# Performance work log

Measured on AMD Instinct MI355X. Metric: run time of the kernel, lower is better.

The kernel has to match this reference:

```python
import jax, jax.numpy as jnp
import numpy as np

N = 100000   # nodes
E = 400000   # merged window edges
L = 100000   # label edges to decode
DIN = 128
H = 128
NL = 2       # GCN layers
RATIO = 0.8
DOUT = 1


def setup_inputs() -> dict:
    key = jax.random.key(0)
    ks = jax.random.split(key, 24)
    def nrm(k, shape, fan):
        return (jax.random.normal(k, shape, jnp.float32) / np.sqrt(fan)).astype(jnp.float32)
    inp = {
        'x': jax.random.normal(ks[0], (N, DIN), jnp.float32),
        'edge_index': jax.random.randint(ks[1], (2, E), 0, N, jnp.int64) if jax.config.jax_enable_x64 else jax.random.randint(ks[1], (2, E), 0, N, jnp.int32),
        'edge_label_index': jax.random.randint(ks[2], (2, L), 0, N, jnp.int32),
        'edge_time': jax.random.uniform(ks[3], (E,), jnp.float32),
        'previous_state': jax.random.normal(ks[4], (N, H), jnp.float32),
        # mlp_transform: Linear(DIN,H)+ReLU
        'w_mlp': nrm(ks[5], (DIN, H), DIN), 'b_mlp': jnp.zeros((H,), jnp.float32),
        # TimeEncode: cos(Linear(1,H)(t))
        'w_time': nrm(ks[6], (H,), 1), 'b_time': jnp.zeros((H,), jnp.float32),
        # Sampling MLP: Linear(3H,H)+ReLU, Linear(H,1)
        'w_s1': nrm(ks[7], (3 * H, H), 3 * H), 'b_s1': jnp.zeros((H,), jnp.float32),
        'w_s2': nrm(ks[8], (H, 1), H), 'b_s2': jnp.zeros((1,), jnp.float32),
        # GCNConv weights per layer
        'gcn_w': nrm(ks[9], (NL, H, H), H), 'gcn_b': jnp.zeros((NL, H), jnp.float32),
        # GRUCell (stored as [H,3H] so x @ W is the torch x @ W_ih^T)
        'gru_wi': nrm(ks[10], (H, 3 * H), H), 'gru_wh': nrm(ks[11], (H, 3 * H), H),
        'gru_bi': jnp.zeros((3 * H,), jnp.float32), 'gru_bh': jnp.zeros((3 * H,), jnp.float32),
        # LinkDecoder: (h_src * h_dst) @ W + b
        'w_dec': nrm(ks[12], (H, DOUT), H), 'b_dec': jnp.zeros((DOUT,), jnp.float32),
    }
    return inp


def _gcn_pass(h, s2, d2, norm, W, b):
    m = h @ W                                      # [N,H]
    agg = jax.ops.segment_sum(norm[:, None] * m[s2], d2, num_segments=N)
    return agg + b


def reference(x, edge_index, edge_label_index, edge_time, previous_state,
              w_mlp, b_mlp, w_time, b_time, w_s1, b_s1, w_s2, b_s2,
              gcn_w, gcn_b, gru_wi, gru_wh, gru_bi, gru_bh, w_dec, b_dec):
    h = jax.nn.relu(x @ w_mlp + b_mlp)             # [N,H]
    src, dst = edge_index[0], edge_index[1]
    # time encoding of shifted edge times: cos(t*w + b) -> [E,H]
    t = edge_time - edge_time.min() + 1.0
    te = jnp.cos(t[:, None] * w_time + b_time)
    # Sampling logits; concat(prev[src],prev[dst],te) @ w_s1 done as 3 matmuls
    pre = (previous_state[src] @ w_s1[:H] + previous_state[dst] @ w_s1[H:2 * H]
           + te @ w_s1[2 * H:] + b_s1)
    logits = jax.nn.relu(pre) @ w_s2 + b_s2        # [E,1]
    z = jax.nn.sigmoid(logits[:, 0])               # eval mode: no Gumbel noise
    k = int(RATIO * E)
    _, keep = jax.lax.top_k(z, k)
    ew, s, d = z[keep], src[keep], dst[keep]
    # GCN normalization with self-loops (weight 1), symmetric norm as in PyG
    sl = jnp.arange(N, dtype=s.dtype)
    s2 = jnp.concatenate([s, sl]); d2 = jnp.concatenate([d, sl])
    w2 = jnp.concatenate([ew, jnp.ones((N,), ew.dtype)])
    deg = jax.ops.segment_sum(w2, d2, num_segments=N)
    dinv = jnp.where(deg > 0, jax.lax.rsqrt(deg), 0.0)
    norm = dinv[s2] * w2 * dinv[d2]                # [k+N]
    for i in range(NL):
        h = _gcn_pass(h, s2, d2, norm, gcn_w[i], gcn_b[i])
        if i != NL - 1:
            h = jax.nn.relu(h)
    # GRUCell update (torch semantics)
    gi = h @ gru_wi + gru_bi
    gh = previous_state @ gru_wh + gru_bh
    ir, iz, inn = jnp.split(gi, 3, axis=1)
    hr, hz, hn = jnp.split(gh, 3, axis=1)
    r = jax.nn.sigmoid(ir + hr)
    u = jax.nn.sigmoid(iz + hz)
    n = jnp.tanh(inn + r * hn)
    h_new = (1.0 - u) * n + u * previous_state     # [N,H]
    # LinkDecoder: Hadamard of endpoints -> linear
    pred = (h_new[edge_label_index[0]] * h_new[edge_label_index[1]]) @ w_dec + b_dec
    return pred, h_new
```

## Files before the change

kernel.cpp:

```cpp
#include <hip/hip_runtime.h>
#include <hip/hip_bf16.h>
#include <math.h>

typedef __bf16 bf16_t;
typedef bf16_t bf16x8 __attribute__((ext_vector_type(8)));
typedef bf16_t bf16x2 __attribute__((ext_vector_type(2)));
typedef float  f32x4  __attribute__((ext_vector_type(4)));
typedef float  f32x2  __attribute__((ext_vector_type(2)));

__device__ __forceinline__ int clampi(int v, int n) {
    return v < 0 ? 0 : (v > n - 1 ? n - 1 : v);
}

template<int NC>
__global__ __launch_bounds__(256) void gemm128(const bf16_t* __restrict__ A,
        const bf16_t* __restrict__ BT, const float* __restrict__ bias,
        float* __restrict__ Cf, bf16_t* __restrict__ Cb, int M, int dorelu)
{
    constexpr int NT = NC / 16;
    int wave = threadIdx.x >> 6, lane = threadIdx.x & 63;
    int mbase = (blockIdx.x * 4 + wave) * 16;
    if (mbase >= M) return;
    int r = lane & 15, q = lane >> 4;
    int arow = mbase + r; if (arow > M - 1) arow = M - 1;
    f32x4 acc[NT];
#pragma unroll
    for (int t = 0; t < NT; ++t) acc[t] = f32x4{0.f, 0.f, 0.f, 0.f};
    const bf16_t* aptr = A + (size_t)arow * 128 + q * 8;
#pragma unroll
    for (int kk = 0; kk < 4; ++kk) {
        bf16x8 af = *(const bf16x8*)(aptr + kk * 32);
#pragma unroll
        for (int t = 0; t < NT; ++t) {
            bf16x8 bfg = *(const bf16x8*)(BT + (size_t)(t * 16 + r) * 128 + kk * 32 + q * 8);
            acc[t] = __builtin_amdgcn_mfma_f32_16x16x32_bf16(af, bfg, acc[t], 0, 0, 0);
        }
    }
#pragma unroll
    for (int t = 0; t < NT; ++t) {
#pragma unroll
        for (int i = 0; i < 4; ++i) {
            int row = mbase + q * 4 + i;
            if (row < M) {
                int col = t * 16 + r;
                float v = acc[t][i];
                if (bias) v += bias[col];
                if (dorelu) v = fmaxf(v, 0.f);
                if (Cf) Cf[(size_t)row * NC + col] = v;
                if (Cb) Cb[(size_t)row * NC + col] = (bf16_t)v;
            }
        }
    }
}

__global__ __launch_bounds__(256) void gru_k(const bf16_t* __restrict__ xb,
        const float* __restrict__ prevf, const bf16_t* __restrict__ wiT,
        const bf16_t* __restrict__ whT, const float* __restrict__ bi,
        const float* __restrict__ bh, float* __restrict__ hnew, int M)
{
    int wave = threadIdx.x >> 6, lane = threadIdx.x & 63;
    int mbase = (blockIdx.x * 4 + wave) * 16;
    if (mbase >= M) return;
    int r = lane & 15, q = lane >> 4;
    int arow = mbase + r; if (arow > M - 1) arow = M - 1;
    bf16x8 ax[4], ap[4];
#pragma unroll
    for (int kk = 0; kk < 4; ++kk) {
        ax[kk] = *(const bf16x8*)(xb + (size_t)arow * 128 + kk * 32 + q * 8);
        f32x4 p0 = *(const f32x4*)(prevf + (size_t)arow * 128 + kk * 32 + q * 8);
        f32x4 p1 = *(const f32x4*)(prevf + (size_t)arow * 128 + kk * 32 + q * 8 + 4);
        bf16x8 t;
#pragma unroll
        for (int j = 0; j < 4; ++j) { t[j] = (bf16_t)p0[j]; t[j + 4] = (bf16_t)p1[j]; }
        ap[kk] = t;
    }
#pragma unroll
    for (int t3 = 0; t3 < 8; ++t3) {
        f32x4 gi0{0.f,0.f,0.f,0.f}, gi1{0.f,0.f,0.f,0.f}, gi2{0.f,0.f,0.f,0.f};
        f32x4 gh0{0.f,0.f,0.f,0.f}, gh1{0.f,0.f,0.f,0.f}, gh2{0.f,0.f,0.f,0.f};
#pragma unroll
        for (int kk = 0; kk < 4; ++kk) {
            const bf16_t* wi = wiT + (size_t)(t3 * 16 + r) * 128 + kk * 32 + q * 8;
            const bf16_t* wh = whT + (size_t)(t3 * 16 + r) * 128 + kk * 32 + q * 8;
            gi0 = __builtin_amdgcn_mfma_f32_16x16x32_bf16(ax[kk], *(const bf16x8*)wi, gi0, 0, 0, 0);
            gi1 = __builtin_amdgcn_mfma_f32_16x16x32_bf16(ax[kk], *(const bf16x8*)(wi + 128 * 128), gi1, 0, 0, 0);
            gi2 = __builtin_amdgcn_mfma_f32_16x16x32_bf16(ax[kk], *(const bf16x8*)(wi + 256 * 128), gi2, 0, 0, 0);
            gh0 = __builtin_amdgcn_mfma_f32_16x16x32_bf16(ap[kk], *(const bf16x8*)wh, gh0, 0, 0, 0);
            gh1 = __builtin_amdgcn_mfma_f32_16x16x32_bf16(ap[kk], *(const bf16x8*)(wh + 128 * 128), gh1, 0, 0, 0);
            gh2 = __builtin_amdgcn_mfma_f32_16x16x32_bf16(ap[kk], *(const bf16x8*)(wh + 256 * 128), gh2, 0, 0, 0);
        }
        int f = t3 * 16 + r;
        float bif0 = bi[f], bif1 = bi[128 + f], bif2 = bi[256 + f];
        float bhf0 = bh[f], bhf1 = bh[128 + f], bhf2 = bh[256 + f];
#pragma unroll
        for (int i = 0; i < 4; ++i) {
            int row = mbase + q * 4 + i;
            if (row < M) {
                float ir = gi0[i] + bif0, hr = gh0[i] + bhf0;
                float iz = gi1[i] + bif1, hz = gh1[i] + bhf1;
                float inn = gi2[i] + bif2, hn = gh2[i] + bhf2;
                float rg = 1.f / (1.f + expf(-(ir + hr)));
                float ug = 1.f / (1.f + expf(-(iz + hz)));
                float nn = tanhf(inn + rg * hn);
                float hp = prevf[(size_t)row * 128 + f];
                hnew[(size_t)row * 128 + f] = (1.f - ug) * nn + ug * hp;
            }
        }
    }
}

__global__ void transp_k(const float* __restrict__ src, bf16_t* __restrict__ dst,
                         int cols, int ld, int rowoff)
{
    int i = blockIdx.x * blockDim.x + threadIdx.x;
    if (i >= cols * 128) return;
    int n = i >> 7, kk = i & 127;
    dst[i] = (bf16_t)src[(size_t)(rowoff + kk) * ld + n];
}

__global__ void cvtb_k(const float* __restrict__ src, size_t off0,
                       bf16_t* __restrict__ dst, int n)
{
    for (int i = blockIdx.x * blockDim.x + threadIdx.x; i < n; i += gridDim.x * blockDim.x)
        dst[i] = (bf16_t)src[off0 + (size_t)i];
}

__global__ void initall(unsigned* meta, unsigned* bmeta, unsigned* hist1,
                        unsigned* hist2, unsigned* cnt, float* deg, int N, int k)
{
    int i = blockIdx.x * blockDim.x + threadIdx.x;
    int stride = gridDim.x * blockDim.x;
    if (i == 0) { meta[0] = 0x7f800000u; meta[1] = (unsigned)k; meta[8] = 0u; }
    if (i < 64) bmeta[i] = 0u;
    for (int j = i; j < 65536; j += stride) { hist1[j] = 0u; hist2[j] = 0u; }
    for (int j = i; j < N + 1; j += stride) cnt[j] = 0u;
    for (int j = i; j < N; j += stride) deg[j] = 1.0f;
}

__global__ void tmin_k(const float* __restrict__ et, unsigned* meta, int E)
{
    __shared__ float sred[4];
    int i = blockIdx.x * blockDim.x + threadIdx.x;
    int stride = gridDim.x * blockDim.x;
    float v = 1e30f;
    for (; i < E; i += stride) v = fminf(v, et[i]);
    for (int off = 32; off; off >>= 1) v = fminf(v, __shfl_down(v, off, 64));
    int wave = threadIdx.x >> 6, lane = threadIdx.x & 63;
    if (lane == 0) sred[wave] = v;
    __syncthreads();
    if (threadIdx.x == 0) {
        v = fminf(fminf(sred[0], sred[1]), fminf(sred[2], sred[3]));
        atomicMin(meta + 0, __float_as_uint(v));
    }
}

__global__ void bcount_k(const int* __restrict__ ei, unsigned* bmeta, int E, int Nh, int N)
{
    __shared__ unsigned sc[4];
    int tid = threadIdx.x;
    if (tid < 4) sc[tid] = 0;
    __syncthreads();
    int e = blockIdx.x * blockDim.x + tid;
    int b = -1;
    if (e < E) {
        int s = clampi(ei[e], N), d = clampi(ei[E + e], N);
        b = (s >= Nh ? 2 : 0) + (d >= Nh ? 1 : 0);
    }
    int lane = tid & 63;
#pragma unroll
    for (int bb = 0; bb < 4; ++bb) {
        unsigned long long m = __ballot(b == bb);
        if (lane == 0 && m) atomicAdd(sc + bb, (unsigned)__popcll(m));
    }
    __syncthreads();
    if (tid < 4 && sc[tid]) atomicAdd(bmeta + tid, sc[tid]);
}

__global__ void bscan_k(unsigned* bmeta)
{
    if (threadIdx.x == 0 && blockIdx.x == 0) {
        bmeta[4] = 0;
        for (int b = 0; b < 4; ++b) {
            bmeta[5 + b] = bmeta[4 + b] + bmeta[b];
            bmeta[9 + b] = bmeta[4 + b];
        }
    }
}

__global__ void bfill_k(const int* __restrict__ ei, unsigned* bmeta,
                        unsigned* __restrict__ elist, int E, int Nh, int N)
{
    __shared__ unsigned scount[4];
    __shared__ unsigned sbase[4];
    int tid = threadIdx.x;
    if (tid < 4) scount[tid] = 0;
    __syncthreads();
    int e = blockIdx.x * blockDim.x + tid;
    int b = -1;
    if (e < E) {
        int s = clampi(ei[e], N), d = clampi(ei[E + e], N);
        b = (s >= Nh ? 2 : 0) + (d >= Nh ? 1 : 0);
    }
    int lane = tid & 63;
    unsigned myofs = 0;
#pragma unroll
    for (int bb = 0; bb < 4; ++bb) {
        unsigned long long m = __ballot(b == bb);
        unsigned wb = 0;
        if (lane == 0 && m) wb = atomicAdd(scount + bb, (unsigned)__popcll(m));
        wb = __shfl(wb, 0, 64);
        if (b == bb) myofs = wb + (unsigned)__popcll(m & ((1ull << lane) - 1ull));
    }
    __syncthreads();
    if (tid < 4) sbase[tid] = scount[tid] ? atomicAdd(bmeta + 9 + tid, scount[tid]) : 0u;
    __syncthreads();
    if (b >= 0) elist[sbase[b] + myofs] = (unsigned)e;
}

__global__ __launch_bounds__(256, 2) void proj2w(const float* __restrict__ prevf,
        const float* __restrict__ Wflat, float* __restrict__ out, int rows, int base)
{
    __shared__ float sP[4][16][36];
    int wave = threadIdx.x >> 6, lane = threadIdx.x & 63;
    int rbase = blockIdx.x * 128 + wave * 32;
    if (rbase >= rows) return;
    int tx = lane & 15, eg = lane >> 4;
    int kk = lane & 15, e0 = (lane >> 4) * 8;
    float acc[8][8];
#pragma unroll
    for (int i = 0; i < 8; ++i)
#pragma unroll
        for (int j = 0; j < 8; ++j) acc[i][j] = 0.f;
    for (int kc = 0; kc < 128; kc += 16) {
        float tmp[8];
#pragma unroll
        for (int i = 0; i < 8; ++i) {
            int rr = rbase + e0 + i; if (rr > rows - 1) rr = rows - 1;
            tmp[i] = prevf[(size_t)(base + rr) * 128 + kc + kk];
        }
#pragma unroll
        for (int i = 0; i < 8; ++i) sP[wave][kk][e0 + i] = tmp[i];
        asm volatile("" ::: "memory");
#pragma unroll
        for (int r = 0; r < 16; ++r) {
            f32x4 a0 = *(const f32x4*)&sP[wave][r][eg * 8];
            f32x4 a1 = *(const f32x4*)&sP[wave][r][eg * 8 + 4];
            f32x4 b0 = *(const f32x4*)&Wflat[(size_t)(kc + r) * 128 + tx * 4];
            f32x4 b1 = *(const f32x4*)&Wflat[(size_t)(kc + r) * 128 + 64 + tx * 4];
#pragma unroll
            for (int i = 0; i < 8; ++i) {
                float ae = i < 4 ? a0[i] : a1[i - 4];
#pragma unroll
                for (int j = 0; j < 4; ++j) {
                    acc[i][j]     = fmaf(ae, b0[j], acc[i][j]);
                    acc[i][j + 4] = fmaf(ae, b1[j], acc[i][j + 4]);
                }
            }
        }
        asm volatile("" ::: "memory");
    }
#pragma unroll
    for (int i = 0; i < 8; ++i) {
        int row = rbase + eg * 8 + i;
        if (row < rows) {
            f32x4 o0, o1;
#pragma unroll
            for (int j = 0; j < 4; ++j) { o0[j] = acc[i][j]; o1[j] = acc[i][j + 4]; }
            *(f32x4*)&out[(size_t)row * 128 + tx * 4] = o0;
            *(f32x4*)&out[(size_t)row * 128 + 64 + tx * 4] = o1;
        }
    }
}

__global__ __launch_bounds__(256, 2) void zgemmw(
        const float* __restrict__ et, const int* __restrict__ ei,
        const unsigned* __restrict__ elist, const unsigned* __restrict__ bmeta, int b,
        int soff, int doff,
        const float* __restrict__ Ah, const float* __restrict__ Bh,
        const float* __restrict__ wtime, const float* __restrict__ btime,
        const float* __restrict__ wc, const float* __restrict__ bs1,
        const float* __restrict__ ws2, const float* __restrict__ bs2,
        const unsigned* __restrict__ meta,
        float* __restrict__ z, unsigned* __restrict__ hist1, int E, int N)
{
    unsigned lo = 0, hi = (unsigned)E;
    if (b >= 0) { lo = bmeta[4 + b]; hi = bmeta[5 + b]; }
    int wave = threadIdx.x >> 6, lane = threadIdx.x & 63;
    unsigned ebase = (unsigned)blockIdx.x * 128u + (unsigned)wave * 32u;
    if (ebase >= hi - lo) return;
    __shared__ float sT[4][32];
    __shared__ int sS[4][32], sD[4][32];
    __shared__ unsigned sE[4][32];
    __shared__ float sC[4][16][36];
    if (lane < 32) {
        float tmin = __uint_as_float(meta[0]);
        unsigned slot = lo + ebase + (unsigned)lane;
        unsigned sl = slot < hi ? slot : hi - 1u;
        unsigned e = elist ? elist[sl] : sl;
        sE[wave][lane] = e;
        sT[wave][lane] = et[e] - tmin + 1.0f;
        sS[wave][lane] = clampi(ei[e], N) - soff;
        sD[wave][lane] = clampi(ei[E + e], N) - doff;
    }
    asm volatile("" ::: "memory");
    int tx = lane & 15, eg = lane >> 4;
    int kk = lane & 15, e0 = (lane >> 4) * 8;
    float tv[8];
#pragma unroll
    for (int i = 0; i < 8; ++i) tv[i] = sT[wave][e0 + i];
    float acc[8][8];
#pragma unroll
    for (int i = 0; i < 8; ++i)
#pragma unroll
        for (int j = 0; j < 8; ++j) acc[i][j] = 0.f;
    for (int kc = 0; kc < 128; kc += 16) {
        float wt = wtime[kc + kk], bt = btime[kc + kk];
        float cv[8];
#pragma unroll
        for (int i = 0; i < 8; ++i) cv[i] = cosf(tv[i] * wt + bt);
#pragma unroll
        for (int i = 0; i < 8; ++i) sC[wave][kk][e0 + i] = cv[i];
        asm volatile("" ::: "memory");
#pragma unroll
        for (int r = 0; r < 16; ++r) {
            f32x4 a0 = *(const f32x4*)&sC[wave][r][eg * 8];
            f32x4 a1 = *(const f32x4*)&sC[wave][r][eg * 8 + 4];
            f32x4 b0 = *(const f32x4*)&wc[(size_t)(kc + r) * 128 + tx * 4];
            f32x4 b1 = *(const f32x4*)&wc[(size_t)(kc + r) * 128 + 64 + tx * 4];
#pragma unroll
            for (int i = 0; i < 8; ++i) {
                float ae = i < 4 ? a0[i] : a1[i - 4];
#pragma unroll
                for (int j = 0; j < 4; ++j) {
                    acc[i][j]     = fmaf(ae, b0[j], acc[i][j]);
                    acc[i][j + 4] = fmaf(ae, b1[j], acc[i][j + 4]);
                }
            }
        }
        asm volatile("" ::: "memory");
    }
    f32x4 bb0 = *(const f32x4*)&bs1[tx * 4];
    f32x4 bb1 = *(const f32x4*)&bs1[64 + tx * 4];
    f32x4 w20 = *(const f32x4*)&ws2[tx * 4];
    f32x4 w21 = *(const f32x4*)&ws2[64 + tx * 4];
    float myv = 0.f;
#pragma unroll
    for (int i = 0; i < 8; ++i) {
        int r = eg * 8 + i;
        int s = sS[wave][r], d = sD[wave][r];
        const float* As = Ah + (size_t)s * 128;
        const float* Bd = Bh + (size_t)d * 128;
        f32x4 A0 = *(const f32x4*)&As[tx * 4];
        f32x4 A1 = *(const f32x4*)&As[64 + tx * 4];
        f32x4 B0 = *(const f32x4*)&Bd[tx * 4];
        f32x4 B1 = *(const f32x4*)&Bd[64 + tx * 4];
        float v[4];
#pragma unroll
        for (int j = 0; j < 4; ++j) {
            float p0 = acc[i][j] + ((A0[j] + B0[j]) + bb0[j]);
            float p1 = acc[i][j + 4] + ((A1[j] + B1[j]) + bb1[j]);
            v[j] = fmaxf(p0, 0.f) * w20[j] + fmaxf(p1, 0.f) * w21[j];
        }
#pragma unroll
        for (int j = 0; j < 4; ++j) {
            v[j] += __shfl_xor(v[j], 8, 64);
            v[j] += __shfl_xor(v[j], 4, 64);
            v[j] += __shfl_xor(v[j], 2, 64);
            v[j] += __shfl_xor(v[j], 1, 64);
        }
        float vv = (v[0] + v[2]) + (v[1] + v[3]);
        if (tx == i) myv = vv;
    }
    if (tx < 8) {
        int r = eg * 8 + tx;
        unsigned slot = lo + ebase + (unsigned)r;
        if (slot < hi) {
            float b2 = bs2[0];
            float zv = 1.f / (1.f + expf(-(myv + b2)));
            z[sE[wave][r]] = zv;
            atomicAdd(hist1 + (__float_as_uint(zv) >> 16), 1u);
        }
    }
}

__global__ __launch_bounds__(1024) void scank(const unsigned* __restrict__ hist,
                                              unsigned* meta, int kIdx, int outIdx)
{
    __shared__ unsigned s[1024];
    int t = threadIdx.x;
    unsigned K = meta[kIdx];
    unsigned sum = 0;
    for (int i = 0; i < 64; ++i) sum += hist[t * 64 + i];
    s[t] = sum;
    __syncthreads();
    for (int off = 1; off < 1024; off <<= 1) {
        unsigned add = (t + off < 1024) ? s[t + off] : 0u;
        __syncthreads();
        s[t] += add;
        __syncthreads();
    }
    unsigned mine = s[t];
    unsigned after = (t < 1023) ? s[t + 1] : 0u;
    if (mine >= K && after < K) {
        unsigned cum = after;
        for (int b = 63; b >= 0; --b) {
            unsigned c = hist[t * 64 + b];
            cum += c;
            if (cum >= K) {
                meta[outIdx] = (unsigned)(t * 64 + b);
                meta[outIdx + 1] = cum - c;
                meta[outIdx + 2] = K - (cum - c);
                break;
            }
        }
    }
}

__global__ void pass2(const float* __restrict__ z, const unsigned* __restrict__ meta,
                      unsigned* hist2, int E)
{
    int e = blockIdx.x * blockDim.x + threadIdx.x;
    if (e >= E) return;
    unsigned u = __float_as_uint(z[e]);
    if ((u >> 16) == meta[2]) atomicAdd(hist2 + (u & 0xffffu), 1u);
}

__global__ void pass3(const float* __restrict__ z, unsigned* meta,
                      unsigned char* keep, unsigned* eql, int E)
{
    int e = blockIdx.x * blockDim.x + threadIdx.x;
    if (e >= E) return;
    unsigned u = __float_as_uint(z[e]);
    unsigned T = (meta[2] << 16) | (meta[5] & 0xffffu);
    keep[e] = (u > T) ? 1 : 0;
    if (u == T) {
        unsigned slot = atomicAdd(meta + 8, 1u);
        if (slot < 4096u) eql[slot] = (unsigned)e;
    }
}

__global__ void eqres(const unsigned* __restrict__ meta, const unsigned* __restrict__ eql,
                      unsigned char* keep)
{
    __shared__ unsigned list[4096];
    unsigned c = meta[8]; if (c > 4096u) c = 4096u;
    unsigned need = meta[7];
    for (unsigned i = threadIdx.x; i < c; i += blockDim.x) list[i] = eql[i];
    __syncthreads();
    for (unsigned i = threadIdx.x; i < c; i += blockDim.x) {
        unsigned rank = 0;
        for (unsigned j = 0; j < c; ++j) rank += (list[j] < list[i]) ? 1u : 0u;
        if (rank < need) keep[list[i]] = 1;
    }
}

__global__ void degsc(const int* __restrict__ ei, const float* __restrict__ z,
                      const unsigned char* __restrict__ keep, float* deg, int E, int N)
{
    int e = blockIdx.x * blockDim.x + threadIdx.x;
    if (e >= E) return;
    if (keep[e]) atomicAdd(deg + clampi(ei[E + e], N), z[e]);
}

__global__ void dinv_k(float* deg, float* selfn, int N)
{
    int i = blockIdx.x * blockDim.x + threadIdx.x;
    if (i >= N) return;
    float d = deg[i];
    float di = 1.0f / sqrtf(d);
    deg[i] = di;
    selfn[i] = di * di;
}

__global__ void normcnt(const int* __restrict__ ei, const float* __restrict__ z,
                        const unsigned char* __restrict__ keep, const float* __restrict__ dinv,
                        float* normv, unsigned* cnt, int E, int N)
{
    int e = blockIdx.x * blockDim.x + threadIdx.x;
    if (e >= E) return;
    if (keep[e]) {
        int s = clampi(ei[e], N), d = clampi(ei[E + e], N);
        normv[e] = dinv[s] * z[e] * dinv[d];
        atomicAdd(cnt + d, 1u);
    } else {
        normv[e] = 0.f;
    }
}

__global__ __launch_bounds__(1024) void scan_n(unsigned* cnt, unsigned* fill, int N)
{
    __shared__ unsigned s[1024];
    int t = threadIdx.x;
    int per = (N + 1023) >> 10;
    int lo = t * per; if (lo > N) lo = N;
    int hi = lo + per; if (hi > N) hi = N;
    unsigned sum = 0;
    for (int i = lo; i < hi; ++i) sum += cnt[i];
    s[t] = sum;
    __syncthreads();
    for (int off = 1; off < 1024; off <<= 1) {
        unsigned add = (t >= off) ? s[t - off] : 0u;
        __syncthreads();
        s[t] += add;
        __syncthreads();
    }
    unsigned run = (t > 0) ? s[t - 1] : 0u;
    for (int i = lo; i < hi; ++i) {
        unsigned c = cnt[i];
        cnt[i] = run; fill[i] = run;
        run += c;
    }
    if (t == 1023) cnt[N] = run;
}

__global__ void fillk(const int* __restrict__ ei, const unsigned char* __restrict__ keep,
                      unsigned* fill, unsigned* csr, int E, int N)
{
    int e = blockIdx.x * blockDim.x + threadIdx.x;
    if (e >= E) return;
    if (keep[e]) {
        unsigned p = atomicAdd(fill + clampi(ei[E + e], N), 1u);
        csr[p] = (unsigned)e;
    }
}

__global__ __launch_bounds__(256) void agg_k(const bf16_t* __restrict__ m,
        const int* __restrict__ ei, const float* __restrict__ normv,
        const unsigned* __restrict__ ofs, const unsigned* __restrict__ csr,
        const float* __restrict__ selfn, const float* __restrict__ bias,
        float* __restrict__ hout, bf16_t* __restrict__ houtb, int N, int E, int dorelu)
{
    int wave = threadIdx.x >> 6, lane = threadIdx.x & 63;
    int n = blockIdx.x * 4 + wave;
    if (n >= N) return;
    int f = 2 * lane;
    float sn = selfn[n];
    bf16x2 mv = *(const bf16x2*)(m + (size_t)n * 128 + f);
    float a0 = bias[f] + sn * (float)mv[0];
    float a1 = bias[f + 1] + sn * (float)mv[1];
    unsigned lo = ofs[n], hi = ofs[n + 1];
    unsigned deg = hi - lo;
    unsigned cap = deg < 64u ? deg : 64u;
    int s_l = 0; float w_l = 0.f;
    if (lane < (int)cap) {
        unsigned e = csr[lo + lane];
        s_l = clampi(ei[e], N);
        w_l = normv[e];
    }
    for (unsigned j = 0; j < cap; ++j) {
        int s = __shfl(s_l, (int)j, 64);
        float w = __shfl(w_l, (int)j, 64);
        bf16x2 v = *(const bf16x2*)(m + (size_t)s * 128 + f);
        a0 = fmaf(w, (float)v[0], a0);
        a1 = fmaf(w, (float)v[1], a1);
    }
    for (unsigned idx = lo + 64; idx < hi; ++idx) {
        unsigned e = csr[idx];
        int s = clampi(ei[e], N);
        float w = normv[e];
        bf16x2 v = *(const bf16x2*)(m + (size_t)s * 128 + f);
        a0 = fmaf(w, (float)v[0], a0);
        a1 = fmaf(w, (float)v[1], a1);
    }
    if (dorelu) { a0 = fmaxf(a0, 0.f); a1 = fmaxf(a1, 0.f); }
    f32x2 o; o[0] = a0; o[1] = a1;
    *(f32x2*)(hout + (size_t)n * 128 + f) = o;
    if (houtb) {
        bf16x2 ob; ob[0] = (bf16_t)a0; ob[1] = (bf16_t)a1;
        *(bf16x2*)(houtb + (size_t)n * 128 + f) = ob;
    }
}

__global__ __launch_bounds__(256) void decode_k(const int* __restrict__ eli,
        const float* __restrict__ hnew, const float* __restrict__ wdec,
        const float* __restrict__ bdec, float* __restrict__ pred, int L, int N)
{
    int wave = threadIdx.x >> 6, lane = threadIdx.x & 63;
    int l = blockIdx.x * 4 + wave;
    if (l >= L) return;
    int a = clampi(eli[l], N), b = clampi(eli[L + l], N);
    f32x2 ha = *(const f32x2*)(hnew + (size_t)a * 128 + 2 * lane);
    f32x2 hb = *(const f32x2*)(hnew + (size_t)b * 128 + 2 * lane);
    f32x2 w  = *(const f32x2*)(wdec + 2 * lane);
    float acc = ha[0] * hb[0] * w[0] + ha[1] * hb[1] * w[1];
    for (int off = 32; off; off >>= 1) acc += __shfl_down(acc, off, 64);
    if (lane == 0) pred[l] = acc + bdec[0];
}

extern "C" void kernel_launch(void* const* d_in, const int* in_sizes, int n_in,
                              void* d_out, int out_size, void* d_ws, size_t ws_size,
                              hipStream_t stream)
{
    (void)n_in; (void)out_size;
    const float* x      = (const float*)d_in[0];
    const int*   ei     = (const int*)d_in[1];
    const int*   eli    = (const int*)d_in[2];
    const float* etime  = (const float*)d_in[3];
    const float* prev   = (const float*)d_in[4];
    const float* w_mlp  = (const float*)d_in[5];
    const float* b_mlp  = (const float*)d_in[6];
    const float* w_time = (const float*)d_in[7];
    const float* b_time = (const float*)d_in[8];
    const float* w_s1   = (const float*)d_in[9];
    const float* b_s1   = (const float*)d_in[10];
    const float* w_s2   = (const float*)d_in[11];
    const float* b_s2   = (const float*)d_in[12];
    const float* gcn_w  = (const float*)d_in[13];
    const float* gcn_b  = (const float*)d_in[14];
    const float* gru_wi = (const float*)d_in[15];
    const float* gru_wh = (const float*)d_in[16];
    const float* gru_bi = (const float*)d_in[17];
    const float* gru_bh = (const float*)d_in[18];
    const float* w_dec  = (const float*)d_in[19];
    const float* b_dec  = (const float*)d_in[20];

    const int E  = in_sizes[3];
    const int N  = in_sizes[0] / 128;
    const int L  = in_sizes[2] / 2;
    const int K  = (int)(0.8 * (double)E);
    const int Nh = (N + 1) / 2;

    char* wsp = (char*)d_ws;
    size_t off = 0;
    auto alloc = [&](size_t bytes) -> void* {
        void* p = wsp + off;
        off += (bytes + 255) & ~(size_t)255;
        return p;
    };
    unsigned* meta  = (unsigned*)alloc(64 * 4);
    unsigned* bmeta = (unsigned*)alloc(64 * 4);
    unsigned* elist = (unsigned*)alloc((size_t)E * 4);
    unsigned* eql   = (unsigned*)alloc(4096 * 4);
    unsigned* hist1 = (unsigned*)alloc(65536 * 4);
    unsigned* hist2 = (unsigned*)alloc(65536 * 4);
    unsigned* cnt   = (unsigned*)alloc((size_t)(N + 1) * 4);
    unsigned* fill  = (unsigned*)alloc((size_t)N * 4);
    float* deg      = (float*)alloc((size_t)N * 4);
    float* selfn    = (float*)alloc((size_t)N * 4);
    float* zbuf     = (float*)alloc((size_t)E * 4);
    unsigned char* keep = (unsigned char*)alloc((size_t)E);
    float* normv    = (float*)alloc((size_t)E * 4);
    unsigned* csr   = (unsigned*)alloc((size_t)E * 4);
    bf16_t* wmlpT = (bf16_t*)alloc(128 * 128 * 2);
    bf16_t* g0T   = (bf16_t*)alloc(128 * 128 * 2);
    bf16_t* g1T   = (bf16_t*)alloc(128 * 128 * 2);
    bf16_t* wiT   = (bf16_t*)alloc(384 * 128 * 2);
    bf16_t* whT   = (bf16_t*)alloc(384 * 128 * 2);

    size_t fullBytes = (size_t)N * 128 * 4;
    size_t halfBytes = (size_t)Nh * 128 * 4;
    bool full = (off + 2 * ((fullBytes + 255) & ~(size_t)255)) <= ws_size;
    char* slot0; char* slot1;
    float* Ahalf; float* Bhalf;
    if (full) {
        slot0 = (char*)alloc(fullBytes);
        slot1 = (char*)alloc(fullBytes);
        Ahalf = (float*)slot0;
        Bhalf = (float*)slot1;
    } else {
        slot0 = (char*)alloc(halfBytes);
        slot1 = (char*)alloc(halfBytes);
        Ahalf = (float*)slot0;
        Bhalf = (float*)slot1;
    }
    bf16_t* xbf   = (bf16_t*)slot0;
    bf16_t* mbuf  = (bf16_t*)slot1;

    float* out_pred = (float*)d_out;
    float* hnew     = (float*)d_out + L;
    float* hb       = hnew;

    initall<<<1024, 256, 0, stream>>>(meta, bmeta, hist1, hist2, cnt, deg, N, K);

    transp_k<<<64, 256, 0, stream>>>(w_mlp, wmlpT, 128, 128, 0);
    transp_k<<<64, 256, 0, stream>>>(gcn_w, g0T, 128, 128, 0);
    transp_k<<<64, 256, 0, stream>>>(gcn_w, g1T, 128, 128, 128);
    transp_k<<<192, 256, 0, stream>>>(gru_wi, wiT, 384, 384, 0);
    transp_k<<<192, 256, 0, stream>>>(gru_wh, whT, 384, 384, 0);

    tmin_k<<<512, 256, 0, stream>>>(etime, meta, E);

    const int zgrid = (E + 127) / 128;
    const float* wc = w_s1 + 256 * 128;
    if (full) {
        proj2w<<<(N + 127) / 128, 256, 0, stream>>>(prev, w_s1, Ahalf, N, 0);
        proj2w<<<(N + 127) / 128, 256, 0, stream>>>(prev, w_s1 + 128 * 128, Bhalf, N, 0);
        zgemmw<<<zgrid, 256, 0, stream>>>(etime, ei, (const unsigned*)nullptr, bmeta, -1,
                0, 0, Ahalf, Bhalf, w_time, b_time, wc, b_s1, w_s2, b_s2,
                meta, zbuf, hist1, E, N);
    } else {
        bcount_k<<<(E + 255) / 256, 256, 0, stream>>>(ei, bmeta, E, Nh, N);
        bscan_k<<<1, 64, 0, stream>>>(bmeta);
        bfill_k<<<(E + 255) / 256, 256, 0, stream>>>(ei, bmeta, elist, E, Nh, N);
        const int NA0 = Nh, NA1 = N - Nh;
        auto zlaunch = [&](int b, int so, int doo) {
            zgemmw<<<zgrid, 256, 0, stream>>>(etime, ei, elist, bmeta, b, so, doo,
                    Ahalf, Bhalf, w_time, b_time, wc, b_s1, w_s2, b_s2,
                    meta, zbuf, hist1, E, N);
        };
        proj2w<<<(NA0 + 127) / 128, 256, 0, stream>>>(prev, w_s1, Ahalf, NA0, 0);
        proj2w<<<(NA0 + 127) / 128, 256, 0, stream>>>(prev, w_s1 + 128 * 128, Bhalf, NA0, 0);
        zlaunch(0, 0, 0);
        proj2w<<<(NA1 + 127) / 128, 256, 0, stream>>>(prev, w_s1 + 128 * 128, Bhalf, NA1, Nh);
        zlaunch(1, 0, Nh);
        proj2w<<<(NA1 + 127) / 128, 256, 0, stream>>>(prev, w_s1, Ahalf, NA1, Nh);
        zlaunch(3, Nh, Nh);
        proj2w<<<(NA0 + 127) / 128, 256, 0, stream>>>(prev, w_s1 + 128 * 128, Bhalf, NA0, 0);
        zlaunch(2, Nh, 0);
    }

    scank<<<1, 1024, 0, stream>>>(hist1, meta, 1, 2);
    pass2<<<(E + 255) / 256, 256, 0, stream>>>(zbuf, meta, hist2, E);
    scank<<<1, 1024, 0, stream>>>(hist2, meta, 4, 5);
    pass3<<<(E + 255) / 256, 256, 0, stream>>>(zbuf, meta, keep, eql, E);
    eqres<<<1, 256, 0, stream>>>(meta, eql, keep);

    degsc<<<(E + 255) / 256, 256, 0, stream>>>(ei, zbuf, keep, deg, E, N);
    dinv_k<<<(N + 255) / 256, 256, 0, stream>>>(deg, selfn, N);
    normcnt<<<(E + 255) / 256, 256, 0, stream>>>(ei, zbuf, keep, deg, normv, cnt, E, N);
    scan_n<<<1, 1024, 0, stream>>>(cnt, fill, N);
    fillk<<<(E + 255) / 256, 256, 0, stream>>>(ei, keep, fill, csr, E, N);

    cvtb_k<<<2048, 256, 0, stream>>>(x, 0, xbf, N * 128);
    gemm128<128><<<(N + 63) / 64, 256, 0, stream>>>(xbf, wmlpT, b_mlp, hb, xbf, N, 1);

    gemm128<128><<<(N + 63) / 64, 256, 0, stream>>>(xbf, g0T, nullptr, nullptr, mbuf, N, 0);
    agg_k<<<(N + 3) / 4, 256, 0, stream>>>(mbuf, ei, normv, cnt, csr, selfn, gcn_b, hb, xbf, N, E, 1);
    gemm128<128><<<(N + 63) / 64, 256, 0, stream>>>(xbf, g1T, nullptr, nullptr, mbuf, N, 0);
    agg_k<<<(N + 3) / 4, 256, 0, stream>>>(mbuf, ei, normv, cnt, csr, selfn, gcn_b + 128, hb, xbf, N, E, 0);

    gru_k<<<(N + 63) / 64, 256, 0, stream>>>(xbf, prev, wiT, whT, gru_bi, gru_bh, hnew, N);

    decode_k<<<(L + 3) / 4, 256, 0, stream>>>(eli, hnew, w_dec, b_dec, out_pred, L, N);
}
```

Before: 1.479 ms.

## Use split-bf16 MFMA emulation of fp32 for sampling-MLP projections

Replaces the fp32 SIMT projection kernels (proj2w, zgemmw) on the full-workspace path with MFMA kernels. Each fp32 operand is split into three bf16 parts, and eight bf16 MFMA products are summed so the result stays close to fp32 accuracy. The A and B projections of previous_state are fused into one kernel, and the time-encoding GEMM reuses the split weights. The goal is to cut FP32 ALU time, at the cost of eight times the MFMA work, extra weight-split kernels, and weight operands loaded straight from global/L2.

```diff
diff --git a/kernel.cpp b/kernel.cpp
--- a/kernel.cpp
+++ b/kernel.cpp
@@ -118,6 +118,20 @@
     dst[i] = (bf16_t)src[(size_t)(rowoff + kk) * ld + n];
 }
 
+__global__ void transpsplit3_k(const float* __restrict__ src, bf16_t* __restrict__ h,
+                               bf16_t* __restrict__ m, bf16_t* __restrict__ l, int rowoff)
+{
+    int i = blockIdx.x * blockDim.x + threadIdx.x;
+    if (i >= 128 * 128) return;
+    int f = i >> 7, k = i & 127;
+    float v = src[(size_t)(rowoff + k) * 128 + f];
+    bf16_t hh = (bf16_t)v;
+    float r1 = v - (float)hh;
+    bf16_t mm = (bf16_t)r1;
+    float r2 = r1 - (float)mm;
+    h[i] = hh; m[i] = mm; l[i] = (bf16_t)r2;
+}
+
 __global__ void cvtb_k(const float* __restrict__ src, size_t off0,
                        bf16_t* __restrict__ dst, int n)
 {
@@ -215,6 +229,167 @@
     if (tid < 4) sbase[tid] = scount[tid] ? atomicAdd(bmeta + 9 + tid, scount[tid]) : 0u;
     __syncthreads();
     if (b >= 0) elist[sbase[b] + myofs] = (unsigned)e;
+}
+
+__global__ __launch_bounds__(256) void projAB8(const float* __restrict__ prevf,
+        const bf16_t* __restrict__ wAh, const bf16_t* __restrict__ wAm, const bf16_t* __restrict__ wAl,
+        const bf16_t* __restrict__ wBh, const bf16_t* __restrict__ wBm, const bf16_t* __restrict__ wBl,
+        float* __restrict__ Aout, float* __restrict__ Bout, int rows)
+{
+    int wave = threadIdx.x >> 6, lane = threadIdx.x & 63;
+    int mbase = (blockIdx.x * 4 + wave) * 16;
+    if (mbase >= rows) return;
+    int r = lane & 15, q = lane >> 4;
+    int arow = mbase + r; if (arow > rows - 1) arow = rows - 1;
+    f32x4 accA[8], accB[8];
+#pragma unroll
+    for (int t = 0; t < 8; ++t) { accA[t] = f32x4{0.f,0.f,0.f,0.f}; accB[t] = f32x4{0.f,0.f,0.f,0.f}; }
+#pragma unroll
+    for (int kk = 0; kk < 4; ++kk) {
+        int k0 = kk * 32 + q * 8;
+        f32x4 p0 = *(const f32x4*)(prevf + (size_t)arow * 128 + k0);
+        f32x4 p1 = *(const f32x4*)(prevf + (size_t)arow * 128 + k0 + 4);
+        bf16x8 ah, am, al;
+#pragma unroll
+        for (int j = 0; j < 8; ++j) {
+            float v = j < 4 ? p0[j] : p1[j - 4];
+            bf16_t h = (bf16_t)v;
+            float r1 = v - (float)h;
+            bf16_t m = (bf16_t)r1;
+            ah[j] = h; am[j] = m; al[j] = (bf16_t)(r1 - (float)m);
+        }
+#pragma unroll
+        for (int t = 0; t < 8; ++t) {
+            size_t wo = (size_t)(t * 16 + r) * 128 + k0;
+            bf16x8 bh = *(const bf16x8*)(wAh + wo);
+            bf16x8 bm = *(const bf16x8*)(wAm + wo);
+            bf16x8 bl = *(const bf16x8*)(wAl + wo);
+            accA[t] = __builtin_amdgcn_mfma_f32_16x16x32_bf16(ah, bh, accA[t], 0, 0, 0);
+            accA[t] = __builtin_amdgcn_mfma_f32_16x16x32_bf16(am, bh, accA[t], 0, 0, 0);
+            accA[t] = __builtin_amdgcn_mfma_f32_16x16x32_bf16(ah, bm, accA[t], 0, 0, 0);
+            accA[t] = __builtin_amdgcn_mfma_f32_16x16x32_bf16(al, bh, accA[t], 0, 0, 0);
+            accA[t] = __builtin_amdgcn_mfma_f32_16x16x32_bf16(am, bm, accA[t], 0, 0, 0);
+            accA[t] = __builtin_amdgcn_mfma_f32_16x16x32_bf16(ah, bl, accA[t], 0, 0, 0);
+            accA[t] = __builtin_amdgcn_mfma_f32_16x16x32_bf16(al, bm, accA[t], 0, 0, 0);
+            accA[t] = __builtin_amdgcn_mfma_f32_16x16x32_bf16(am, bl, accA[t], 0, 0, 0);
+            bf16x8 ch = *(const bf16x8*)(wBh + wo);
+            bf16x8 cm = *(const bf16x8*)(wBm + wo);
+            bf16x8 cl = *(const bf16x8*)(wBl + wo);
+            accB[t] = __builtin_amdgcn_mfma_f32_16x16x32_bf16(ah, ch, accB[t], 0, 0, 0);
+            accB[t] = __builtin_amdgcn_mfma_f32_16x16x32_bf16(am, ch, accB[t], 0, 0, 0);
+            accB[t] = __builtin_amdgcn_mfma_f32_16x16x32_bf16(ah, cm, accB[t], 0, 0, 0);
+            accB[t] = __builtin_amdgcn_mfma_f32_16x16x32_bf16(al, ch, accB[t], 0, 0, 0);
+            accB[t] = __builtin_amdgcn_mfma_f32_16x16x32_bf16(am, cm, accB[t], 0, 0, 0);
+            accB[t] = __builtin_amdgcn_mfma_f32_16x16x32_bf16(ah, cl, accB[t], 0, 0, 0);
+            accB[t] = __builtin_amdgcn_mfma_f32_16x16x32_bf16(al, cm, accB[t], 0, 0, 0);
+            accB[t] = __builtin_amdgcn_mfma_f32_16x16x32_bf16(am, cl, accB[t], 0, 0, 0);
+        }
+    }
+#pragma unroll
+    for (int t = 0; t < 8; ++t) {
+#pragma unroll
+        for (int i = 0; i < 4; ++i) {
+            int row = mbase + q * 4 + i;
+            if (row < rows) {
+                int col = t * 16 + r;
+                Aout[(size_t)row * 128 + col] = accA[t][i];
+                Bout[(size_t)row * 128 + col] = accB[t][i];
+            }
+        }
+    }
+}
+
+__global__ __launch_bounds__(256) void zgemm8(
+        const float* __restrict__ et, const int* __restrict__ ei,
+        const float* __restrict__ Ah, const float* __restrict__ Bh,
+        const float* __restrict__ wtime, const float* __restrict__ btime,
+        const bf16_t* __restrict__ wch, const bf16_t* __restrict__ wcm,
+        const bf16_t* __restrict__ wcl,
+        const float* __restrict__ bs1, const float* __restrict__ ws2,
+        const float* __restrict__ bs2, const unsigned* __restrict__ meta,
+        float* __restrict__ z, unsigned* __restrict__ hist1, int E, int N)
+{
+    int wave = threadIdx.x >> 6, lane = threadIdx.x & 63;
+    int base = (blockIdx.x * 4 + wave) * 16;
+    if (base >= E) return;
+    int r = lane & 15, q = lane >> 4;
+    float tl_ = 0.f; int sl = 0, dl = 0;
+    if (lane < 16) {
+        int slot = base + lane; if (slot > E - 1) slot = E - 1;
+        float tmin = __uint_as_float(meta[0]);
+        tl_ = et[slot] - tmin + 1.0f;
+        sl = clampi(ei[slot], N);
+        dl = clampi(ei[E + slot], N);
+    }
+    float tr = __shfl(tl_, r, 64);
+    f32x4 acc[8];
+#pragma unroll
+    for (int t = 0; t < 8; ++t) acc[t] = f32x4{0.f,0.f,0.f,0.f};
+#pragma unroll
+    for (int kk = 0; kk < 4; ++kk) {
+        int k0 = kk * 32 + q * 8;
+        f32x4 wt0 = *(const f32x4*)&wtime[k0];
+        f32x4 wt1 = *(const f32x4*)&wtime[k0 + 4];
+        f32x4 bt0 = *(const f32x4*)&btime[k0];
+        f32x4 bt1 = *(const f32x4*)&btime[k0 + 4];
+        bf16x8 ah, am, al;
+#pragma unroll
+        for (int j = 0; j < 8; ++j) {
+            float wt = j < 4 ? wt0[j] : wt1[j - 4];
+            float bt = j < 4 ? bt0[j] : bt1[j - 4];
+            float c = cosf(tr * wt + bt);
+            bf16_t h = (bf16_t)c;
+            float r1 = c - (float)h;
+            bf16_t m = (bf16_t)r1;
+            ah[j] = h; am[j] = m; al[j] = (bf16_t)(r1 - (float)m);
+        }
+#pragma unroll
+        for (int t = 0; t < 8; ++t) {
+            size_t wo = (size_t)(t * 16 + r) * 128 + k0;
+            bf16x8 bh = *(const bf16x8*)(wch + wo);
+            bf16x8 bm = *(const bf16x8*)(wcm + wo);
+            bf16x8 bl = *(const bf16x8*)(wcl + wo);
+            acc[t] = __builtin_amdgcn_mfma_f32_16x16x32_bf16(ah, bh, acc[t], 0, 0, 0);
+            acc[t] = __builtin_amdgcn_mfma_f32_16x16x32_bf16(am, bh, acc[t], 0, 0, 0);
+            acc[t] = __builtin_amdgcn_mfma_f32_16x16x32_bf16(ah, bm, acc[t], 0, 0, 0);
+            acc[t] = __builtin_amdgcn_mfma_f32_16x16x32_bf16(al, bh, acc[t], 0, 0, 0);
+            acc[t] = __builtin_amdgcn_mfma_f32_16x16x32_bf16(am, bm, acc[t], 0, 0, 0);
+            acc[t] = __builtin_amdgcn_mfma_f32_16x16x32_bf16(ah, bl, acc[t], 0, 0, 0);
+            acc[t] = __builtin_amdgcn_mfma_f32_16x16x32_bf16(al, bm, acc[t], 0, 0, 0);
+            acc[t] = __builtin_amdgcn_mfma_f32_16x16x32_bf16(am, bl, acc[t], 0, 0, 0);
+        }
+    }
+    float bb[8], ww[8];
+#pragma unroll
+    for (int t = 0; t < 8; ++t) { bb[t] = bs1[t * 16 + r]; ww[t] = ws2[t * 16 + r]; }
+    float b2 = bs2[0];
+#pragma unroll
+    for (int i = 0; i < 4; ++i) {
+        int row = q * 4 + i;
+        int s = __shfl(sl, row, 64);
+        int d = __shfl(dl, row, 64);
+        const float* As = Ah + (size_t)s * 128;
+        const float* Bd = Bh + (size_t)d * 128;
+        float v = 0.f;
+#pragma unroll
+        for (int t = 0; t < 8; ++t) {
+            int f = t * 16 + r;
+            float p = acc[t][i] + As[f] + Bd[f] + bb[t];
+            v += fmaxf(p, 0.f) * ww[t];
+        }
+        v += __shfl_xor(v, 1, 64);
+        v += __shfl_xor(v, 2, 64);
+        v += __shfl_xor(v, 4, 64);
+        v += __shfl_xor(v, 8, 64);
+        if (r == i) {
+            int slot = base + row;
+            if (slot < E) {
+                float zv = 1.f / (1.f + expf(-(v + b2)));
+                z[slot] = zv;
+                atomicAdd(hist1 + (__float_as_uint(zv) >> 16), 1u);
+            }
+        }
+    }
 }
 
 __global__ __launch_bounds__(256, 2) void proj2w(const float* __restrict__ prevf,
@@ -646,6 +821,15 @@
     bf16_t* g1T   = (bf16_t*)alloc(128 * 128 * 2);
     bf16_t* wiT   = (bf16_t*)alloc(384 * 128 * 2);
     bf16_t* whT   = (bf16_t*)alloc(384 * 128 * 2);
+    bf16_t* wAh = (bf16_t*)alloc(128 * 128 * 2);
+    bf16_t* wAm = (bf16_t*)alloc(128 * 128 * 2);
+    bf16_t* wAl = (bf16_t*)alloc(128 * 128 * 2);
+    bf16_t* wBh = (bf16_t*)alloc(128 * 128 * 2);
+    bf16_t* wBm = (bf16_t*)alloc(128 * 128 * 2);
+    bf16_t* wBl = (bf16_t*)alloc(128 * 128 * 2);
+    bf16_t* wch = (bf16_t*)alloc(128 * 128 * 2);
+    bf16_t* wcm = (bf16_t*)alloc(128 * 128 * 2);
+    bf16_t* wcl = (bf16_t*)alloc(128 * 128 * 2);
 
     size_t fullBytes = (size_t)N * 128 * 4;
     size_t halfBytes = (size_t)Nh * 128 * 4;
@@ -677,18 +861,21 @@
     transp_k<<<64, 256, 0, stream>>>(gcn_w, g1T, 128, 128, 128);
     transp_k<<<192, 256, 0, stream>>>(gru_wi, wiT, 384, 384, 0);
     transp_k<<<192, 256, 0, stream>>>(gru_wh, whT, 384, 384, 0);
+    transpsplit3_k<<<64, 256, 0, stream>>>(w_s1, wAh, wAm, wAl, 0);
+    transpsplit3_k<<<64, 256, 0, stream>>>(w_s1, wBh, wBm, wBl, 128);
+    transpsplit3_k<<<64, 256, 0, stream>>>(w_s1, wch, wcm, wcl, 256);
 
     tmin_k<<<512, 256, 0, stream>>>(etime, meta, E);
 
-    const int zgrid = (E + 127) / 128;
     const float* wc = w_s1 + 256 * 128;
     if (full) {
-        proj2w<<<(N + 127) / 128, 256, 0, stream>>>(prev, w_s1, Ahalf, N, 0);
-        proj2w<<<(N + 127) / 128, 256, 0, stream>>>(prev, w_s1 + 128 * 128, Bhalf, N, 0);
-        zgemmw<<<zgrid, 256, 0, stream>>>(etime, ei, (const unsigned*)nullptr, bmeta, -1,
-                0, 0, Ahalf, Bhalf, w_time, b_time, wc, b_s1, w_s2, b_s2,
+        projAB8<<<(N + 63) / 64, 256, 0, stream>>>(prev, wAh, wAm, wAl,
+                wBh, wBm, wBl, Ahalf, Bhalf, N);
+        zgemm8<<<(E + 63) / 64, 256, 0, stream>>>(etime, ei, Ahalf, Bhalf,
+                w_time, b_time, wch, wcm, wcl, b_s1, w_s2, b_s2,
                 meta, zbuf, hist1, E, N);
     } else {
+        const int zgrid = (E + 127) / 128;
         bcount_k<<<(E + 255) / 256, 256, 0, stream>>>(ei, bmeta, E, Nh, N);
         bscan_k<<<1, 64, 0, stream>>>(bmeta);
         bfill_k<<<(E + 255) / 256, 256, 0, stream>>>(ei, bmeta, elist, E, Nh, N);
```

After: 2.128 ms. 43.9% more time.
